# Performance work log

Measured on AMD Instinct MI355X. Metric: run time of the kernel, lower is better.

The kernel has to match this reference:

```python
import jax, jax.numpy as jnp
import numpy as np

B_, L_, DM, DS, DC, EX = 4, 2048, 1024, 16, 4, 2
DI = DM * EX

def setup_inputs() -> dict:
    key = jax.random.key(0)
    ks = jax.random.split(key, 8)
    s = lambda i, shape, scale: jax.random.normal(ks[i], shape, jnp.float32) * scale
    return dict(
        x=s(0, (B_, L_, DM), 1.0),
        in_proj_w=s(1, (2 * DI, DM), 0.02),
        conv_weight=s(2, (DI, DC), 0.1),
        conv_bias=jnp.zeros((DI,), jnp.float32),
        A_log=jax.random.uniform(ks[3], (DS,), jnp.float32, -4.0, -1.0),
        D=jnp.ones((DI,), jnp.float32),
        delta_w=s(4, (DS, DI), 0.02),
        delta_b=jnp.ones((DS,), jnp.float32),
        B_w=s(5, (DS, DI), 0.02),
        C_w=s(6, (DS, DI), 0.02),
        out_proj_w=s(7, (DM, DI), 0.02),
    )

def reference(x, in_proj_w, conv_weight, conv_bias, A_log, D, delta_w, delta_b, B_w, C_w, out_proj_w):
    Bb, L, Dm = x.shape
    di, dc = conv_weight.shape
    # 1. input projection and split into ssm / gate branches
    x_inner = x @ in_proj_w.T                       # [B,L,2*di]
    x_ssm, x_gate = x_inner[..., :di], x_inner[..., di:]
    # 2. causal depthwise conv1d + SiLU (kernel size dc, per-channel weights)
    xp = jnp.pad(x_ssm, ((0, 0), (dc - 1, 0), (0, 0)))
    xc = conv_bias + sum(xp[:, k:k + L, :] * conv_weight[:, k] for k in range(dc))
    x_conv = jax.nn.silu(xc)                         # [B,L,di]
    # 3. content-aware discretization
    delta = jax.nn.softplus(x_conv @ delta_w.T + delta_b)  # [B,L,N]
    Bs = x_conv @ B_w.T                              # [B,L,N]
    Cs = x_conv @ C_w.T                              # [B,L,N]
    A = -jnp.exp(A_log)                              # [N]
    xavg = x_conv.mean(axis=-1)                      # [B,L]
    # 4. selective SSM scan over L with state h:[B,N]
    def step(h, inp):
        dt, bt, ct, xa = inp                         # [B,N],[B,N],[B,N],[B]
        h = jnp.exp(dt * A) * h + dt * bt * xa[:, None]
        return h, (h * ct).sum(-1)                   # y_t: [B]
    h0 = jnp.zeros((Bb, A.shape[0]), x.dtype)
    _, ys = jax.lax.scan(
        step, h0,
        (delta.transpose(1, 0, 2), Bs.transpose(1, 0, 2), Cs.transpose(1, 0, 2), xavg.T))
    y_ssm = ys.T[..., None]                          # [B,L,1] (broadcasts over di)
    # 5. gate, skip, output projection
    y_gated = y_ssm * jax.nn.silu(x_gate)
    y_skip = y_gated + x_conv * D
    return y_skip @ out_proj_w.T                     # [B,L,D]
```

## Files before the change

kernel.cpp:

```cpp
#include <hip/hip_runtime.h>
#include <cmath>

#define LL 2048
#define NROW 8192
#define DMODEL 1024
#define DINNER 2048
#define NSTATE 16
#define NSEG 256
#define SEGLEN 8

typedef unsigned short u16;
typedef __attribute__((ext_vector_type(8))) unsigned short u16x8;
typedef __attribute__((ext_vector_type(8))) short short8;
typedef __attribute__((ext_vector_type(4))) float floatx4;
typedef __attribute__((ext_vector_type(16))) float floatx16;

__device__ __forceinline__ float bf2f(u16 h) {
    unsigned u = ((unsigned)h) << 16;
    float f;
    __builtin_memcpy(&f, &u, 4);
    return f;
}
__device__ __forceinline__ u16 f2bf(float f) {
    unsigned u;
    __builtin_memcpy(&u, &f, 4);
    u = u + 0x7fffu + ((u >> 16) & 1u);
    return (u16)(u >> 16);
}
__device__ __forceinline__ float silu_f(float x) { return x / (1.f + __expf(-x)); }

__global__ __launch_bounds__(256) void cvt_multi(
    const float* __restrict__ s0, const float* __restrict__ s1,
    const float* __restrict__ s2, const float* __restrict__ s3,
    const float* __restrict__ s4, const float* __restrict__ s5,
    u16* __restrict__ d0, u16* __restrict__ d1, u16* __restrict__ d2,
    u16* __restrict__ d3, u16* __restrict__ d4, u16* __restrict__ d5) {
    int bid = blockIdx.x;
    const float* s;
    u16* d;
    size_t off;
    if (bid < 4096)      { s = s0; d = d0; off = (size_t)bid * 2048; }
    else if (bid < 6144) { s = s1; d = d1; off = (size_t)(bid - 4096) * 2048; }
    else if (bid < 7168) { s = s2; d = d2; off = (size_t)(bid - 6144) * 2048; }
    else if (bid < 7184) { s = s3; d = d3; off = (size_t)(bid - 7168) * 2048; }
    else if (bid < 7200) { s = s4; d = d4; off = (size_t)(bid - 7184) * 2048; }
    else                 { s = s5; d = d5; off = (size_t)(bid - 7200) * 2048; }
    size_t i = off + (size_t)threadIdx.x * 8;
    float4 a = *(const float4*)&s[i];
    float4 b = *(const float4*)&s[i + 4];
    u16x8 o;
    o[0] = f2bf(a.x); o[1] = f2bf(a.y); o[2] = f2bf(a.z); o[3] = f2bf(a.w);
    o[4] = f2bf(b.x); o[5] = f2bf(b.y); o[6] = f2bf(b.z); o[7] = f2bf(b.w);
    *(u16x8*)&d[i] = o;
}

template <int OUT_BF16>
__global__ __launch_bounds__(256) void gemm_bt_mfma(
    const u16* __restrict__ A, const u16* __restrict__ B,
    void* __restrict__ Cout, int N, int K) {
    __shared__ u16 As[128 * 32];
    __shared__ u16 Bs[128 * 32];
    const int tid = threadIdx.x;
    const int lane = tid & 63;
    const int wave = tid >> 6;
    const int bm = blockIdx.y * 128;
    const int bn = blockIdx.x * 128;

    const int srow = lane >> 2;
    const u16* ag[2];
    const u16* bg[2];
#pragma unroll
    for (int p = 0; p < 2; ++p) {
        int c = wave * 2 + p;
        int kbg = (lane & 3) ^ ((srow >> 1) & 3) ^ (2 * (p & 1));
        ag[p] = A + (size_t)(bm + c * 16 + srow) * K + kbg * 8;
        bg[p] = B + (size_t)(bn + c * 16 + srow) * K + kbg * 8;
    }
    const int frow = lane & 31;
    const int khi = lane >> 5;
    const int wr = (wave >> 1) * 64;
    const int wc = (wave & 1) * 64;
    const int fswz = ((frow >> 1) & 3) ^ (2 * ((frow >> 4) & 1));
    int aoff[2][2], boff[2][2];
#pragma unroll
    for (int mi = 0; mi < 2; ++mi)
#pragma unroll
        for (int kh = 0; kh < 2; ++kh) {
            int rA = wr + mi * 32 + frow;
            int rB = wc + mi * 32 + frow;
            int kb = kh * 2 + khi;
            aoff[mi][kh] = rA * 32 + (kb ^ fswz) * 8;
            boff[mi][kh] = rB * 32 + (kb ^ fswz) * 8;
        }
    floatx16 acc[2][2];
#pragma unroll
    for (int i = 0; i < 2; ++i)
#pragma unroll
        for (int j = 0; j < 2; ++j) acc[i][j] = (floatx16)(0.f);

    for (int k0 = 0; k0 < K; k0 += 32) {
        __syncthreads();
#pragma unroll
        for (int p = 0; p < 2; ++p) {
            int c = wave * 2 + p;
            __builtin_amdgcn_global_load_lds(
                (const __attribute__((address_space(1))) void*)ag[p],
                (__attribute__((address_space(3))) void*)&As[c * 512], 16, 0, 0);
            __builtin_amdgcn_global_load_lds(
                (const __attribute__((address_space(1))) void*)bg[p],
                (__attribute__((address_space(3))) void*)&Bs[c * 512], 16, 0, 0);
            ag[p] += 32;
            bg[p] += 32;
        }
        __syncthreads();
        short8 af[2][2], bf[2][2];
#pragma unroll
        for (int mi = 0; mi < 2; ++mi)
#pragma unroll
            for (int kh = 0; kh < 2; ++kh) {
                af[mi][kh] = *(const short8*)&As[aoff[mi][kh]];
                bf[mi][kh] = *(const short8*)&Bs[boff[mi][kh]];
            }
#pragma unroll
        for (int kh = 0; kh < 2; ++kh)
#pragma unroll
            for (int mi = 0; mi < 2; ++mi)
#pragma unroll
                for (int ni = 0; ni < 2; ++ni)
                    acc[mi][ni] = __builtin_amdgcn_mfma_f32_32x32x16_bf16(
                        af[mi][kh], bf[ni][kh], acc[mi][ni], 0, 0, 0);
    }
    const int cc = lane & 31;
    const int rbase = 4 * (lane >> 5);
#pragma unroll
    for (int mi = 0; mi < 2; ++mi)
#pragma unroll
        for (int ni = 0; ni < 2; ++ni)
#pragma unroll
            for (int r = 0; r < 16; ++r) {
                int grow = bm + wr + mi * 32 + (r & 3) + 8 * (r >> 2) + rbase;
                int gcol = bn + wc + ni * 32 + cc;
                float v = acc[mi][ni][r];
                if (OUT_BF16)
                    ((u16*)Cout)[(size_t)grow * N + gcol] = f2bf(v);
                else
                    ((float*)Cout)[(size_t)grow * N + gcol] = v;
            }
}

__global__ __launch_bounds__(256) void conv_silu_avg(
    const u16* __restrict__ xin, const float* __restrict__ cw,
    const float* __restrict__ cb, u16* __restrict__ xconv,
    float* __restrict__ xavg) {
    const int blk = blockIdx.x;
    const int b = blk >> 7;
    const int lc = blk & 127;
    const int row0 = b * LL + lc * 16;
    const int tid = threadIdx.x;
    const int lane = tid & 63, wave = tid >> 6;
    const int d0 = tid * 8;
    float4 cwv[8];
    float cbv[8];
#pragma unroll
    for (int e = 0; e < 8; ++e) cwv[e] = *(const float4*)&cw[(d0 + e) * 4];
#pragma unroll
    for (int e = 0; e < 8; e += 4) {
        float4 c = *(const float4*)&cb[d0 + e];
        cbv[e] = c.x; cbv[e + 1] = c.y; cbv[e + 2] = c.z; cbv[e + 3] = c.w;
    }
    u16x8 w0, w1, w2;
    if (lc == 0) {
        w0 = (u16x8)0; w1 = (u16x8)0; w2 = (u16x8)0;
    } else {
        w0 = *(const u16x8*)&xin[(size_t)(row0 - 3) * (2 * DINNER) + d0];
        w1 = *(const u16x8*)&xin[(size_t)(row0 - 2) * (2 * DINNER) + d0];
        w2 = *(const u16x8*)&xin[(size_t)(row0 - 1) * (2 * DINNER) + d0];
    }
    float sums[16];
#pragma unroll
    for (int t = 0; t < 16; ++t) {
        u16x8 cur = *(const u16x8*)&xin[(size_t)(row0 + t) * (2 * DINNER) + d0];
        float lsum = 0.f;
        u16x8 o;
#pragma unroll
        for (int e = 0; e < 8; ++e) {
            float acc = cbv[e];
            acc += bf2f(w0[e]) * cwv[e].x;
            acc += bf2f(w1[e]) * cwv[e].y;
            acc += bf2f(w2[e]) * cwv[e].z;
            acc += bf2f(cur[e]) * cwv[e].w;
            float s = silu_f(acc);
            lsum += s;
            o[e] = f2bf(s);
        }
        *(u16x8*)&xconv[(size_t)(row0 + t) * DINNER + d0] = o;
        sums[t] = lsum;
        w0 = w1; w1 = w2; w2 = cur;
    }
#pragma unroll
    for (int off = 32; off; off >>= 1)
#pragma unroll
        for (int t = 0; t < 16; ++t) sums[t] += __shfl_down(sums[t], off);
    __shared__ float wred[4][16];
    if (lane == 0) {
#pragma unroll
        for (int t = 0; t < 16; ++t) wred[wave][t] = sums[t];
    }
    __syncthreads();
    if (tid < 16)
        xavg[row0 + tid] = (wred[0][tid] + wred[1][tid] + wred[2][tid] + wred[3][tid]) *
                           (1.f / DINNER);
}

__global__ __launch_bounds__(256) void dbc_mfma(
    const u16* __restrict__ xconv, const u16* __restrict__ wcat,
    const float* __restrict__ db, const float* __restrict__ A_log,
    const float* __restrict__ xavg,
    float* __restrict__ a_out, float* __restrict__ u_out, float* __restrict__ c_out) {
    __shared__ u16 As[128 * 32];
    __shared__ u16 Bs[48 * 32];
    const int tid = threadIdx.x;
    const int lane = tid & 63;
    const int wave = tid >> 6;
    const int bm = blockIdx.x * 128;

    const int kbg = (lane & 3) ^ ((lane >> 3) & 3);
    const int srow = lane >> 2;
    const u16* ag[2];
#pragma unroll
    for (int p = 0; p < 2; ++p) {
        int c = wave * 2 + p;
        ag[p] = xconv + (size_t)(bm + c * 16 + srow) * DINNER + kbg * 8;
    }
    const u16* bgp = wcat + (size_t)(wave * 16 + srow) * DINNER + kbg * 8;
    const int fr = lane & 15;
    const int kb = lane >> 4;
    const int kbs = kb ^ ((fr >> 1) & 3);
    int aoff[2], boff[3];
#pragma unroll
    for (int mi = 0; mi < 2; ++mi) aoff[mi] = (wave * 32 + mi * 16 + fr) * 32 + kbs * 8;
#pragma unroll
    for (int ni = 0; ni < 3; ++ni) boff[ni] = (ni * 16 + fr) * 32 + kbs * 8;

    floatx4 acc[2][3];
#pragma unroll
    for (int mi = 0; mi < 2; ++mi)
#pragma unroll
        for (int ni = 0; ni < 3; ++ni) acc[mi][ni] = (floatx4){0.f, 0.f, 0.f, 0.f};

    for (int k0 = 0; k0 < DINNER; k0 += 32) {
        __syncthreads();
#pragma unroll
        for (int p = 0; p < 2; ++p) {
            int c = wave * 2 + p;
            __builtin_amdgcn_global_load_lds(
                (const __attribute__((address_space(1))) void*)ag[p],
                (__attribute__((address_space(3))) void*)&As[c * 512], 16, 0, 0);
            ag[p] += 32;
        }
        if (wave < 3) {
            __builtin_amdgcn_global_load_lds(
                (const __attribute__((address_space(1))) void*)bgp,
                (__attribute__((address_space(3))) void*)&Bs[wave * 512], 16, 0, 0);
            bgp += 32;
        }
        __syncthreads();
        short8 af[2], bf[3];
#pragma unroll
        for (int mi = 0; mi < 2; ++mi) af[mi] = *(const short8*)&As[aoff[mi]];
#pragma unroll
        for (int ni = 0; ni < 3; ++ni) bf[ni] = *(const short8*)&Bs[boff[ni]];
#pragma unroll
        for (int mi = 0; mi < 2; ++mi)
#pragma unroll
            for (int ni = 0; ni < 3; ++ni)
                acc[mi][ni] = __builtin_amdgcn_mfma_f32_16x16x32_bf16(af[mi], bf[ni],
                                                                      acc[mi][ni], 0, 0, 0);
    }
    const int cr = (lane >> 4) * 4;
    const int s = lane & 15;
    const float Aa = -__expf(A_log[s]);
    const float dbs = db[s];
#pragma unroll
    for (int mi = 0; mi < 2; ++mi)
#pragma unroll
        for (int r = 0; r < 4; ++r) {
            int row = bm + wave * 32 + mi * 16 + cr + r;
            float pre = acc[mi][0][r] + dbs;
            float delta = (pre > 20.f) ? pre : log1pf(__expf(pre));
            a_out[row * NSTATE + s] = __expf(delta * Aa);
            u_out[row * NSTATE + s] = delta * acc[mi][1][r] * xavg[row];
            c_out[row * NSTATE + s] = acc[mi][2][r];
        }
}

__global__ __launch_bounds__(256) void scan_p1(
    const float* __restrict__ a, const float* __restrict__ u,
    float* __restrict__ Pc, float* __restrict__ H0c) {
    int gid = blockIdx.x * 256 + threadIdx.x;
    int s = gid & 15, seg = (gid >> 4) & (NSEG - 1), b = gid >> 12;
    size_t base = (size_t)(b * LL + seg * SEGLEN) * NSTATE + s;
    float P = 1.f, h = 0.f;
#pragma unroll
    for (int t = 0; t < SEGLEN; ++t) {
        float av = a[base + (size_t)t * NSTATE];
        float uv = u[base + (size_t)t * NSTATE];
        h = fmaf(av, h, uv);
        P *= av;
    }
    int o = (b * NSEG + seg) * NSTATE + s;
    Pc[o] = P;
    H0c[o] = h;
}

__global__ __launch_bounds__(64) void scan_p2(
    const float* __restrict__ Pc, const float* __restrict__ H0c,
    float* __restrict__ hstart) {
    int lane = threadIdx.x;
    int b = lane >> 4, s = lane & 15;
    float h = 0.f;
#pragma unroll 8
    for (int seg = 0; seg < NSEG; ++seg) {
        int o = (b * NSEG + seg) * NSTATE + s;
        hstart[o] = h;
        h = fmaf(Pc[o], h, H0c[o]);
    }
}

__global__ __launch_bounds__(256) void scan_p3(
    const float* __restrict__ a, const float* __restrict__ u,
    const float* __restrict__ c, const float* __restrict__ hstart,
    float* __restrict__ y) {
    int gid = blockIdx.x * 256 + threadIdx.x;
    int s = gid & 15, seg = (gid >> 4) & (NSEG - 1), b = gid >> 12;
    float h = hstart[(b * NSEG + seg) * NSTATE + s];
    size_t base = (size_t)(b * LL + seg * SEGLEN) * NSTATE + s;
#pragma unroll
    for (int t = 0; t < SEGLEN; ++t) {
        float av = a[base + (size_t)t * NSTATE];
        float uv = u[base + (size_t)t * NSTATE];
        float cv = c[base + (size_t)t * NSTATE];
        h = fmaf(av, h, uv);
        float p = h * cv;
        p += __shfl_xor(p, 1);
        p += __shfl_xor(p, 2);
        p += __shfl_xor(p, 4);
        p += __shfl_xor(p, 8);
        if (s == 0) y[b * LL + seg * SEGLEN + t] = p;
    }
}

__global__ __launch_bounds__(256) void gate_skip(
    const u16* __restrict__ xin, const float* __restrict__ y,
    const float* __restrict__ Dv, const u16* __restrict__ xconv,
    u16* __restrict__ yskip) {
    size_t i = ((size_t)blockIdx.x * 256 + threadIdx.x) * 8;
    int row = (int)(i >> 11);
    int d = (int)(i & (DINNER - 1));
    u16x8 g = *(const u16x8*)&xin[(size_t)row * (2 * DINNER) + DINNER + d];
    u16x8 xc = *(const u16x8*)&xconv[i];
    float yv = y[row];
    u16x8 o;
#pragma unroll
    for (int e = 0; e < 8; ++e) {
        float gv = silu_f(bf2f(g[e]));
        float v = yv * gv + bf2f(xc[e]) * Dv[d + e];
        o[e] = f2bf(v);
    }
    *(u16x8*)&yskip[i] = o;
}

extern "C" void kernel_launch(void* const* d_in, const int* in_sizes, int n_in,
                              void* d_out, int out_size, void* d_ws, size_t ws_size,
                              hipStream_t stream) {
    const float* x       = (const float*)d_in[0];
    const float* w_in    = (const float*)d_in[1];
    const float* conv_w  = (const float*)d_in[2];
    const float* conv_b  = (const float*)d_in[3];
    const float* A_log   = (const float*)d_in[4];
    const float* Dv      = (const float*)d_in[5];
    const float* delta_w = (const float*)d_in[6];
    const float* delta_b = (const float*)d_in[7];
    const float* B_w     = (const float*)d_in[8];
    const float* C_w     = (const float*)d_in[9];
    const float* out_w   = (const float*)d_in[10];
    float* out = (float*)d_out;

    u16* xb  = (u16*)d_ws;
    u16* wb  = xb + 8388608;
    u16* owb = wb + 4194304;
    u16* wsb = owb + 2097152;
    u16* xin = wsb + 98304;
    u16* xcv = xin + 33554432;
    u16* ysk = xcv + 16777216;
    float* fb     = (float*)(ysk + 16777216);
    float* abuf   = fb;
    float* ubuf   = abuf + 131072;
    float* cbuf   = ubuf + 131072;
    float* pbuf   = cbuf + 131072;
    float* h0buf  = pbuf + 16384;
    float* hsbuf  = h0buf + 16384;
    float* ybuf   = hsbuf + 16384;
    float* avgbuf = ybuf + 8192;

    cvt_multi<<<7216, 256, 0, stream>>>(x, w_in, out_w, delta_w, B_w, C_w,
                                        xb, wb, owb, wsb, wsb + 32768, wsb + 65536);

    gemm_bt_mfma<1><<<dim3(32, 64), 256, 0, stream>>>(xb, wb, xin, 2 * DINNER, DMODEL);

    conv_silu_avg<<<512, 256, 0, stream>>>(xin, conv_w, conv_b, xcv, avgbuf);
    dbc_mfma<<<64, 256, 0, stream>>>(xcv, wsb, delta_b, A_log, avgbuf,
                                     abuf, ubuf, cbuf);

    scan_p1<<<64, 256, 0, stream>>>(abuf, ubuf, pbuf, h0buf);
    scan_p2<<<1, 64, 0, stream>>>(pbuf, h0buf, hsbuf);
    scan_p3<<<64, 256, 0, stream>>>(abuf, ubuf, cbuf, hsbuf, ybuf);

    gate_skip<<<NROW * DINNER / 8 / 256, 256, 0, stream>>>(xin, ybuf, Dv, xcv, ysk);

    gemm_bt_mfma<0><<<dim3(8, 64), 256, 0, stream>>>(ysk, owb, out, DMODEL, DINNER);
}
```

Baseline: 347.9 us.

## Split-K the output projection with atomics and shrink dbc tiles for more blocks

The output projection GEMM is split along K into two halves launched over a third grid dimension. Each half accumulates into a pre-zeroed fp32 output with atomic adds, which doubles the block count from 512 to 1024 to better fill the GPU. The dbc GEMM moves from 64 blocks of 128 rows to 256 blocks of 32 rows with 128 threads, for more parallelism on that skinny GEMM. In exchange there is an extra zeroing kernel, atomic traffic on the output, and floating-point summation order that is no longer deterministic.

```diff
diff --git a/kernel.cpp b/kernel.cpp
--- a/kernel.cpp
+++ b/kernel.cpp
@@ -54,10 +54,15 @@
     *(u16x8*)&d[i] = o;
 }
 
-template <int OUT_BF16>
+__global__ __launch_bounds__(256) void zero_f4(float* __restrict__ p) {
+    size_t i = ((size_t)blockIdx.x * 256 + threadIdx.x) * 4;
+    *(float4*)&p[i] = make_float4(0.f, 0.f, 0.f, 0.f);
+}
+
+template <int MODE>
 __global__ __launch_bounds__(256) void gemm_bt_mfma(
     const u16* __restrict__ A, const u16* __restrict__ B,
-    void* __restrict__ Cout, int N, int K) {
+    void* __restrict__ Cout, int N, int Kstride, int Kiter) {
     __shared__ u16 As[128 * 32];
     __shared__ u16 Bs[128 * 32];
     const int tid = threadIdx.x;
@@ -65,6 +70,7 @@
     const int wave = tid >> 6;
     const int bm = blockIdx.y * 128;
     const int bn = blockIdx.x * 128;
+    const int kbase = blockIdx.z * Kiter;
 
     const int srow = lane >> 2;
     const u16* ag[2];
@@ -73,8 +79,8 @@
     for (int p = 0; p < 2; ++p) {
         int c = wave * 2 + p;
         int kbg = (lane & 3) ^ ((srow >> 1) & 3) ^ (2 * (p & 1));
-        ag[p] = A + (size_t)(bm + c * 16 + srow) * K + kbg * 8;
-        bg[p] = B + (size_t)(bn + c * 16 + srow) * K + kbg * 8;
+        ag[p] = A + (size_t)(bm + c * 16 + srow) * Kstride + kbase + kbg * 8;
+        bg[p] = B + (size_t)(bn + c * 16 + srow) * Kstride + kbase + kbg * 8;
     }
     const int frow = lane & 31;
     const int khi = lane >> 5;
@@ -98,7 +104,7 @@
 #pragma unroll
         for (int j = 0; j < 2; ++j) acc[i][j] = (floatx16)(0.f);
 
-    for (int k0 = 0; k0 < K; k0 += 32) {
+    for (int k0 = 0; k0 < Kiter; k0 += 32) {
         __syncthreads();
 #pragma unroll
         for (int p = 0; p < 2; ++p) {
@@ -141,10 +147,12 @@
                 int grow = bm + wr + mi * 32 + (r & 3) + 8 * (r >> 2) + rbase;
                 int gcol = bn + wc + ni * 32 + cc;
                 float v = acc[mi][ni][r];
-                if (OUT_BF16)
+                if (MODE == 1)
                     ((u16*)Cout)[(size_t)grow * N + gcol] = f2bf(v);
+                else if (MODE == 0)
+                    ((float*)Cout)[(size_t)grow * N + gcol] = v;
                 else
-                    ((float*)Cout)[(size_t)grow * N + gcol] = v;
+                    unsafeAtomicAdd(&((float*)Cout)[(size_t)grow * N + gcol], v);
             }
 }
 
@@ -212,86 +220,80 @@
                            (1.f / DINNER);
 }
 
-__global__ __launch_bounds__(256) void dbc_mfma(
+__global__ __launch_bounds__(128) void dbc_mfma(
     const u16* __restrict__ xconv, const u16* __restrict__ wcat,
     const float* __restrict__ db, const float* __restrict__ A_log,
     const float* __restrict__ xavg,
     float* __restrict__ a_out, float* __restrict__ u_out, float* __restrict__ c_out) {
-    __shared__ u16 As[128 * 32];
+    __shared__ u16 As[32 * 32];
     __shared__ u16 Bs[48 * 32];
     const int tid = threadIdx.x;
     const int lane = tid & 63;
     const int wave = tid >> 6;
-    const int bm = blockIdx.x * 128;
+    const int bm = blockIdx.x * 32;
 
     const int kbg = (lane & 3) ^ ((lane >> 3) & 3);
     const int srow = lane >> 2;
-    const u16* ag[2];
-#pragma unroll
-    for (int p = 0; p < 2; ++p) {
-        int c = wave * 2 + p;
-        ag[p] = xconv + (size_t)(bm + c * 16 + srow) * DINNER + kbg * 8;
-    }
-    const u16* bgp = wcat + (size_t)(wave * 16 + srow) * DINNER + kbg * 8;
+    const u16* ag  = xconv + (size_t)(bm + wave * 16 + srow) * DINNER + kbg * 8;
+    const u16* bg0 = wcat + (size_t)srow * DINNER + kbg * 8;
+    const u16* bg1 = wcat + (size_t)(16 + srow) * DINNER + kbg * 8;
+    const u16* bg2 = wcat + (size_t)(32 + srow) * DINNER + kbg * 8;
     const int fr = lane & 15;
     const int kb = lane >> 4;
     const int kbs = kb ^ ((fr >> 1) & 3);
-    int aoff[2], boff[3];
-#pragma unroll
-    for (int mi = 0; mi < 2; ++mi) aoff[mi] = (wave * 32 + mi * 16 + fr) * 32 + kbs * 8;
+    const int aoff = (wave * 16 + fr) * 32 + kbs * 8;
+    int boff[3];
 #pragma unroll
     for (int ni = 0; ni < 3; ++ni) boff[ni] = (ni * 16 + fr) * 32 + kbs * 8;
 
-    floatx4 acc[2][3];
-#pragma unroll
-    for (int mi = 0; mi < 2; ++mi)
-#pragma unroll
-        for (int ni = 0; ni < 3; ++ni) acc[mi][ni] = (floatx4){0.f, 0.f, 0.f, 0.f};
+    floatx4 acc[3];
+#pragma unroll
+    for (int ni = 0; ni < 3; ++ni) acc[ni] = (floatx4){0.f, 0.f, 0.f, 0.f};
 
     for (int k0 = 0; k0 < DINNER; k0 += 32) {
         __syncthreads();
-#pragma unroll
-        for (int p = 0; p < 2; ++p) {
-            int c = wave * 2 + p;
+        __builtin_amdgcn_global_load_lds(
+            (const __attribute__((address_space(1))) void*)ag,
+            (__attribute__((address_space(3))) void*)&As[wave * 512], 16, 0, 0);
+        ag += 32;
+        if (wave == 0) {
             __builtin_amdgcn_global_load_lds(
-                (const __attribute__((address_space(1))) void*)ag[p],
-                (__attribute__((address_space(3))) void*)&As[c * 512], 16, 0, 0);
-            ag[p] += 32;
-        }
-        if (wave < 3) {
+                (const __attribute__((address_space(1))) void*)bg0,
+                (__attribute__((address_space(3))) void*)&Bs[0], 16, 0, 0);
+            bg0 += 32;
             __builtin_amdgcn_global_load_lds(
-                (const __attribute__((address_space(1))) void*)bgp,
-                (__attribute__((address_space(3))) void*)&Bs[wave * 512], 16, 0, 0);
-            bgp += 32;
+                (const __attribute__((address_space(1))) void*)bg2,
+                (__attribute__((address_space(3))) void*)&Bs[1024], 16, 0, 0);
+            bg2 += 32;
+        } else {
+            __builtin_amdgcn_global_load_lds(
+                (const __attribute__((address_space(1))) void*)bg1,
+                (__attribute__((address_space(3))) void*)&Bs[512], 16, 0, 0);
+            bg1 += 32;
         }
         __syncthreads();
-        short8 af[2], bf[3];
-#pragma unroll
-        for (int mi = 0; mi < 2; ++mi) af[mi] = *(const short8*)&As[aoff[mi]];
+        short8 af = *(const short8*)&As[aoff];
+        short8 bf[3];
 #pragma unroll
         for (int ni = 0; ni < 3; ++ni) bf[ni] = *(const short8*)&Bs[boff[ni]];
 #pragma unroll
-        for (int mi = 0; mi < 2; ++mi)
-#pragma unroll
-            for (int ni = 0; ni < 3; ++ni)
-                acc[mi][ni] = __builtin_amdgcn_mfma_f32_16x16x32_bf16(af[mi], bf[ni],
-                                                                      acc[mi][ni], 0, 0, 0);
+        for (int ni = 0; ni < 3; ++ni)
+            acc[ni] = __builtin_amdgcn_mfma_f32_16x16x32_bf16(af, bf[ni],
+                                                              acc[ni], 0, 0, 0);
     }
     const int cr = (lane >> 4) * 4;
     const int s = lane & 15;
     const float Aa = -__expf(A_log[s]);
     const float dbs = db[s];
 #pragma unroll
-    for (int mi = 0; mi < 2; ++mi)
-#pragma unroll
-        for (int r = 0; r < 4; ++r) {
-            int row = bm + wave * 32 + mi * 16 + cr + r;
-            float pre = acc[mi][0][r] + dbs;
-            float delta = (pre > 20.f) ? pre : log1pf(__expf(pre));
-            a_out[row * NSTATE + s] = __expf(delta * Aa);
-            u_out[row * NSTATE + s] = delta * acc[mi][1][r] * xavg[row];
-            c_out[row * NSTATE + s] = acc[mi][2][r];
-        }
+    for (int r = 0; r < 4; ++r) {
+        int row = bm + wave * 16 + cr + r;
+        float pre = acc[0][r] + dbs;
+        float delta = (pre > 20.f) ? pre : log1pf(__expf(pre));
+        a_out[row * NSTATE + s] = __expf(delta * Aa);
+        u_out[row * NSTATE + s] = delta * acc[1][r] * xavg[row];
+        c_out[row * NSTATE + s] = acc[2][r];
+    }
 }
 
 __global__ __launch_bounds__(256) void scan_p1(
@@ -406,11 +408,12 @@
     cvt_multi<<<7216, 256, 0, stream>>>(x, w_in, out_w, delta_w, B_w, C_w,
                                         xb, wb, owb, wsb, wsb + 32768, wsb + 65536);
 
-    gemm_bt_mfma<1><<<dim3(32, 64), 256, 0, stream>>>(xb, wb, xin, 2 * DINNER, DMODEL);
+    gemm_bt_mfma<1><<<dim3(32, 64, 1), 256, 0, stream>>>(xb, wb, xin,
+                                                         2 * DINNER, DMODEL, DMODEL);
 
     conv_silu_avg<<<512, 256, 0, stream>>>(xin, conv_w, conv_b, xcv, avgbuf);
-    dbc_mfma<<<64, 256, 0, stream>>>(xcv, wsb, delta_b, A_log, avgbuf,
-                                     abuf, ubuf, cbuf);
+    dbc_mfma<<<256, 128, 0, stream>>>(xcv, wsb, delta_b, A_log, avgbuf,
+                                      abuf, ubuf, cbuf);
 
     scan_p1<<<64, 256, 0, stream>>>(abuf, ubuf, pbuf, h0buf);
     scan_p2<<<1, 64, 0, stream>>>(pbuf, h0buf, hsbuf);
@@ -418,5 +421,7 @@
 
     gate_skip<<<NROW * DINNER / 8 / 256, 256, 0, stream>>>(xin, ybuf, Dv, xcv, ysk);
 
-    gemm_bt_mfma<0><<<dim3(8, 64), 256, 0, stream>>>(ysk, owb, out, DMODEL, DINNER);
-}
+    zero_f4<<<NROW * DMODEL / 4 / 256, 256, 0, stream>>>(out);
+    gemm_bt_mfma<2><<<dim3(8, 64, 2), 256, 0, stream>>>(ysk, owb, out,
+                                                        DMODEL, DINNER, DMODEL);
+}
```

Result: slower. 384.9 us (+10.6%).
